# Kernel optimization log

Hardware: AMD Instinct MI355X
Metric: run time of the kernel (lower is better)

Reference implementation:

```python
import jax, jax.numpy as jnp
import numpy as np

D_MODEL = 512
N_LAYERS = 6
N_HEADS = 8
INNER = 2048
VOCAB = 2048
SEQ = 128
BATCH = 256
HEAD_DIM = D_MODEL // N_HEADS
EPS = 1e-5


def _pos_encoding(seq_len, d_model):
    pos = jnp.arange(seq_len, dtype=jnp.float32)[:, None]          # [S,1]
    i = jnp.arange(d_model // 2, dtype=jnp.float32)[None, :]       # [1,d/2]
    theta = pos / jnp.power(10000.0, 2.0 * i / d_model)            # [S,d/2]
    # interleave sin at even indices, cos at odd indices
    return jnp.stack([jnp.sin(theta), jnp.cos(theta)], axis=-1).reshape(seq_len, d_model)


def _layer_norm_2d(x):
    # F.layer_norm(x, (N, dims)): normalize over last TWO dims, no affine
    m = jnp.mean(x, axis=(1, 2), keepdims=True)
    v = jnp.mean(jnp.square(x - m), axis=(1, 2), keepdims=True)
    return (x - m) / jnp.sqrt(v + EPS)


def setup_inputs() -> dict:
    key = jax.random.key(0)
    ks = jax.random.split(key, 12)
    s = 0.02
    x = jax.random.randint(ks[0], (BATCH, SEQ), 0, VOCAB)
    emb = jax.random.normal(ks[1], (VOCAB, D_MODEL), jnp.float32) * s
    Wq = jax.random.normal(ks[2], (N_LAYERS, N_HEADS, D_MODEL, HEAD_DIM), jnp.float32) * s
    bq = jax.random.normal(ks[3], (N_LAYERS, N_HEADS, HEAD_DIM), jnp.float32) * s
    Wk = jax.random.normal(ks[4], (N_LAYERS, N_HEADS, D_MODEL, HEAD_DIM), jnp.float32) * s
    bk = jax.random.normal(ks[5], (N_LAYERS, N_HEADS, HEAD_DIM), jnp.float32) * s
    Wv = jax.random.normal(ks[6], (N_LAYERS, N_HEADS, D_MODEL, HEAD_DIM), jnp.float32) * s
    bv = jax.random.normal(ks[7], (N_LAYERS, N_HEADS, HEAD_DIM), jnp.float32) * s
    W1 = jax.random.normal(ks[8], (N_LAYERS, D_MODEL, INNER), jnp.float32) * s
    b1 = jax.random.normal(ks[9], (N_LAYERS, INNER), jnp.float32) * s
    W2 = jax.random.normal(ks[10], (N_LAYERS, INNER, D_MODEL), jnp.float32) * s
    b2 = jax.random.normal(ks[11], (N_LAYERS, D_MODEL), jnp.float32) * s
    return {"x": x, "emb": emb, "Wq": Wq, "bq": bq, "Wk": Wk, "bk": bk,
            "Wv": Wv, "bv": bv, "W1": W1, "b1": b1, "W2": W2, "b2": b2}


def reference(x, emb, Wq, bq, Wk, bk, Wv, bv, W1, b1, W2, b2):
    B, S = x.shape
    pe = _pos_encoding(SEQ, D_MODEL)
    h = emb[x] + pe[None, :, :]                                     # [B,S,D]
    scale = HEAD_DIM ** -0.5
    for l in range(N_LAYERS):
        q = jnp.einsum('bsd,hde->bhse', h, Wq[l]) + bq[l][None, :, None, :]
        k = jnp.einsum('bsd,hde->bhse', h, Wk[l]) + bk[l][None, :, None, :]
        v = jnp.einsum('bsd,hde->bhse', h, Wv[l]) + bv[l][None, :, None, :]
        scores = jnp.einsum('bhse,bhte->bhst', q, k) * scale        # no softmax!
        attn = jnp.einsum('bhst,bhte->bhse', scores, v)             # [B,H,S,E]
        attn = jnp.transpose(attn, (0, 2, 1, 3)).reshape(B, S, D_MODEL)
        h = _layer_norm_2d(h + attn)
        ff = jax.nn.relu(h @ W1[l] + b1[l]) @ W2[l] + b2[l]
        h = _layer_norm_2d(h + ff)
    return h
```

## Files before the change

kernel.cpp:

```cpp
#include <hip/hip_runtime.h>
#include <stdint.h>

#define NLAYERS 6
#define DMODEL  512
#define NHEADS  8
#define HDIM    64
#define INNER   2048
#define SEQ     128
#define BATCH   256
#define NTOK    (BATCH*SEQ)

typedef __attribute__((ext_vector_type(4))) float f32x4;
typedef __attribute__((ext_vector_type(8))) _Float16 hfrag;

typedef const __attribute__((address_space(1))) void* gas1p;
typedef __attribute__((address_space(3))) void* las3p;

__device__ __forceinline__ void load_lds16(const void* g, void* l) {
  __builtin_amdgcn_global_load_lds((gas1p)(uintptr_t)g, (las3p)(uint32_t)(uintptr_t)l, 16, 0, 0);
}

__device__ __forceinline__ ushort f2h(float f) {
  return __builtin_bit_cast(ushort, (_Float16)f);
}
__device__ __forceinline__ float h2f(ushort u) {
  return (float)__builtin_bit_cast(_Float16, u);
}

__device__ __forceinline__ f32x4 mfma16(hfrag a, hfrag b, f32x4 c) {
  return __builtin_amdgcn_mfma_f32_16x16x32_f16(a, b, c, 0, 0, 0);
}


__global__ void prep_qkv(const float* __restrict__ Wq, const float* __restrict__ Wk,
                         const float* __restrict__ Wv, const float* __restrict__ bq,
                         const float* __restrict__ bk, const float* __restrict__ bv,
                         ushort* __restrict__ Wt, float* __restrict__ biasq) {
  int idx = blockIdx.x*256 + threadIdx.x;
  if (idx >= NLAYERS*1536*512) return;
  const int k = idx & 511;
  const int n = (idx >> 9) % 1536;
  const int l = idx / (1536*512);
  const int which = n >> 9, hh = (n >> 6) & 7, e = n & 63;
  const float* W = (which == 0) ? Wq : ((which == 1) ? Wk : Wv);
  Wt[idx] = f2h(W[(((size_t)l*NHEADS + hh)*DMODEL + k)*HDIM + e]);
  if (k == 0) {
    const float* bb = (which == 0) ? bq : ((which == 1) ? bk : bv);
    biasq[l*1536 + n] = bb[((size_t)l*NHEADS + hh)*HDIM + e];
  }
}

__global__ void prep_w1(const float* __restrict__ W1, ushort* __restrict__ W1t) {
  int idx = blockIdx.x*256 + threadIdx.x;
  if (idx >= NLAYERS*INNER*512) return;
  const int k = idx & 511;
  const int n = (idx >> 9) % INNER;
  const int l = idx / (INNER*512);
  W1t[idx] = f2h(W1[((size_t)l*DMODEL + k)*INNER + n]);
}

__global__ void prep_w2(const float* __restrict__ W2, ushort* __restrict__ W2t) {
  int idx = blockIdx.x*256 + threadIdx.x;
  if (idx >= NLAYERS*512*INNER) return;
  const int k = idx & 2047;
  const int n = (idx >> 11) & 511;
  const int l = idx / (512*INNER);
  W2t[idx] = f2h(W2[((size_t)l*INNER + k)*DMODEL + n]);
}


__global__ void embed_kernel(const int* __restrict__ x, const float* __restrict__ emb,
                             ushort* __restrict__ hb) {
  const int t = blockIdx.x;
  const int i = threadIdx.x;
  const int s = t & (SEQ-1);
  const int tok = x[t];
  const float freq = expf(-(float)i * (9.210340371976184f / 256.0f));
  const float th = (float)s * freq;
  const float sn = sinf(th), cs = cosf(th);
  const size_t base = (size_t)t*DMODEL;
  const float v0 = emb[(size_t)tok*DMODEL + 2*i]     + sn;
  const float v1 = emb[(size_t)tok*DMODEL + 2*i + 1] + cs;
  *(uint*)(hb + base + 2*i) = (uint)f2h(v0) | ((uint)f2h(v1) << 16);
}


template<int K, int EPI>
__global__ __launch_bounds__(512, 2) void gemm256(
    const ushort* __restrict__ A, const ushort* __restrict__ Bt,
    const float* __restrict__ bias, ushort* __restrict__ outb,
    const int ldc, const int nbn) {
  __shared__ __align__(16) char lds[98304];
  constexpr int NKT = K / 32;
  constexpr int NG  = 2 * NKT;
  const int t = threadIdx.x;
  const int lane = t & 63, w = t >> 6;
  const int wr = w >> 2, wc = w & 3;
  const int cpx = (int)gridDim.x >> 3;
  const int wg  = ((int)blockIdx.x & 7) * cpx + ((int)blockIdx.x >> 3);
  const int bm = wg / nbn, bn = wg % nbn;

  const int fr = lane & 15;
  const int cxor = (((lane >> 4) ^ ((fr >> 1) & 3)) << 4);

  float bias_r[4];
  #pragma unroll
  for (int n = 0; n < 4; ++n) bias_r[n] = bias[bn*256 + wc*64 + n*16 + fr];
  asm volatile("" : "+v"(bias_r[0]), "+v"(bias_r[1]), "+v"(bias_r[2]), "+v"(bias_r[3]));

  const int srow = t >> 2;
  const int scc  = (t & 3) ^ ((t >> 3) & 3);
  const ushort* aSrc = A  + ((size_t)bm*256 + srow)*K + scc*8;
  const ushort* bSrc = Bt + ((size_t)bn*256 + srow)*K + scc*8;

  auto stage_g = [&](int g) {
    const int kt = g >> 1;
    const ushort* src = ((g & 1) ? bSrc : aSrc) + kt*32;
    char* dst = lds + (g % 6)*16384 + t*16;
    load_lds16(src, dst);
    load_lds16(src + (size_t)128*K, dst + 8192);
  };

  f32x4 acc[8][4] = {};

  stage_g(0); stage_g(1); stage_g(2); stage_g(3); stage_g(4);
  asm volatile("s_waitcnt vmcnt(6)" ::: "memory");
  __builtin_amdgcn_s_barrier();

  #pragma unroll 1
  for (int kt = 0; kt < NKT; ++kt) {
    const int Ab = ((2*kt) % 6) * 16384;
    hfrag a[8], b[4];
    #pragma unroll
    for (int m = 0; m < 8; ++m)
      a[m] = *(const hfrag*)(lds + Ab + (wr*128 + m*16 + fr)*64 + cxor);
    #pragma unroll
    for (int n = 0; n < 4; ++n)
      b[n] = *(const hfrag*)(lds + Ab + 16384 + (wc*64 + n*16 + fr)*64 + cxor);
    if (2*kt + 5 < NG) stage_g(2*kt + 5);
    __builtin_amdgcn_s_barrier();
    __builtin_amdgcn_s_setprio(1);
    #pragma unroll
    for (int m = 0; m < 4; ++m)
      #pragma unroll
      for (int n = 0; n < 4; ++n)
        acc[m][n] = mfma16(a[m], b[n], acc[m][n]);
    __builtin_amdgcn_s_setprio(0);
    __builtin_amdgcn_s_barrier();
    if (2*kt + 6 < NG) stage_g(2*kt + 6);
    __builtin_amdgcn_s_barrier();
    __builtin_amdgcn_s_setprio(1);
    #pragma unroll
    for (int m = 4; m < 8; ++m)
      #pragma unroll
      for (int n = 0; n < 4; ++n)
        acc[m][n] = mfma16(a[m], b[n], acc[m][n]);
    __builtin_amdgcn_s_setprio(0);
    if (kt < NKT - 3) {
      asm volatile("s_waitcnt vmcnt(6)" ::: "memory");
    } else if (kt == NKT - 3) {
      asm volatile("s_waitcnt vmcnt(4)" ::: "memory");
    } else if (kt == NKT - 2) {
      asm volatile("s_waitcnt vmcnt(0)" ::: "memory");
    }
    __builtin_amdgcn_s_barrier();
  }

  #pragma unroll
  for (int m = 0; m < 8; ++m) {
    #pragma unroll
    for (int n = 0; n < 4; ++n) {
      #pragma unroll
      for (int r4 = 0; r4 < 4; ++r4) {
        const int row = bm*256 + wr*128 + m*16 + ((lane >> 4) << 2) + r4;
        const int col = bn*256 + wc*64 + n*16 + fr;
        float v = acc[m][n][r4] + bias_r[n];
        if constexpr (EPI == 1) v = fmaxf(v, 0.0f);
        outb[(size_t)row*ldc + col] = f2h(v);
      }
    }
  }
}


__global__ __launch_bounds__(256) void attn_kernel(
    const ushort* __restrict__ qkv, ushort* __restrict__ outb) {
  __shared__ __align__(16) ushort wbuf[4][8192];
  const int tid = threadIdx.x;
  const int w = tid >> 6, lane = tid & 63;
  const int bh = blockIdx.x*4 + w;
  const int b = bh >> 3, h = bh & 7;
  const ushort* tokbase = qkv + (size_t)b*SEQ*1536;
  ushort* lds = &wbuf[w][0];
  ushort* kch = lds;
  ushort* vch = lds + 2048;

  f32x4 acc1[4][4] = {};
  #pragma unroll 1
  for (int sb = 0; sb < 4; ++sb) {
    const int s0 = sb*32;
    const int sr = lane >> 1;
    #pragma unroll
    for (int i = 0; i < 4; ++i) {
      const int cc  = i*2 + (lane & 1);
      const int ccs = cc ^ (sr & 7);
      const ushort* g = tokbase + (size_t)(s0+sr)*1536 + h*64 + cc*8;
      *(uint4*)(kch + sr*64 + ccs*8) = *(const uint4*)(g + 512);
      *(uint4*)(vch + sr*64 + ccs*8) = *(const uint4*)(g + 1024);
    }
    hfrag ak[4], av[4];
    #pragma unroll
    for (int m = 0; m < 4; ++m) {
      const int e1 = m*16 + (lane & 15);
      const int ccb = e1 >> 3, el = e1 & 7;
      #pragma unroll
      for (int j = 0; j < 8; ++j) {
        const int s = (lane >> 4)*8 + j;
        ak[m][j] = __builtin_bit_cast(_Float16, kch[s*64 + ((ccb ^ (s & 7))*8) + el]);
        av[m][j] = __builtin_bit_cast(_Float16, vch[s*64 + ((ccb ^ (s & 7))*8) + el]);
      }
    }
    #pragma unroll
    for (int m = 0; m < 4; ++m)
      #pragma unroll
      for (int n = 0; n < 4; ++n)
        acc1[m][n] = mfma16(ak[m], av[n], acc1[m][n]);
  }

  ushort* tv = lds;
  #pragma unroll
  for (int m = 0; m < 4; ++m)
    #pragma unroll
    for (int n = 0; n < 4; ++n)
      #pragma unroll
      for (int r4 = 0; r4 < 4; ++r4) {
        const int e1 = m*16 + (lane >> 4)*4 + r4;
        const int e2 = n*16 + (lane & 15);
        tv[e2*72 + e1] = f2h(acc1[m][n][r4] * 0.125f);
      }

  f32x4 acc2[8][4] = {};
  #pragma unroll
  for (int eb = 0; eb < 2; ++eb) {
    const int e1b = eb*32 + (lane >> 4)*8;
    hfrag aq[8], bk2[4];
    #pragma unroll
    for (int m = 0; m < 8; ++m) {
      const int s = m*16 + (lane & 15);
      aq[m] = *(const hfrag*)(tokbase + (size_t)s*1536 + h*64 + e1b);
    }
    #pragma unroll
    for (int n = 0; n < 4; ++n) {
      const int e2 = n*16 + (lane & 15);
      bk2[n] = *(const hfrag*)(tv + e2*72 + e1b);
    }
    #pragma unroll
    for (int m = 0; m < 8; ++m)
      #pragma unroll
      for (int n = 0; n < 4; ++n)
        acc2[m][n] = mfma16(aq[m], bk2[n], acc2[m][n]);
  }
  #pragma unroll
  for (int m = 0; m < 8; ++m)
    #pragma unroll
    for (int n = 0; n < 4; ++n)
      #pragma unroll
      for (int r4 = 0; r4 < 4; ++r4) {
        const int s  = m*16 + (lane >> 4)*4 + r4;
        const int e2 = n*16 + (lane & 15);
        outb[((size_t)b*SEQ + s)*DMODEL + h*HDIM + e2] = f2h(acc2[m][n][r4]);
      }
}


template<bool FINAL>
__global__ __launch_bounds__(1024) void resid_ln(
    const ushort* __restrict__ delta, ushort* __restrict__ hb, float* __restrict__ hf) {
  const int b = blockIdx.x;
  const size_t base = (size_t)b * (SEQ*DMODEL);
  uint4 cache[8];
  float s = 0.f, q = 0.f;
  #pragma unroll
  for (int j = 0; j < 8; ++j) {
    const size_t idx = base + (size_t)j*8192 + threadIdx.x*8;
    const uint4 hv = *(const uint4*)(hb + idx);
    const uint4 dv = *(const uint4*)(delta + idx);
    uint4 cv;
    #pragma unroll
    for (int c = 0; c < 4; ++c) {
      const uint hu = (&hv.x)[c], du = (&dv.x)[c];
      const float v0 = h2f((ushort)(hu & 0xffffu)) + h2f((ushort)(du & 0xffffu));
      const float v1 = h2f((ushort)(hu >> 16))     + h2f((ushort)(du >> 16));
      s += v0 + v1; q += v0*v0 + v1*v1;
      (&cv.x)[c] = (uint)f2h(v0) | ((uint)f2h(v1) << 16);
    }
    cache[j] = cv;
  }
  #pragma unroll
  for (int off = 32; off > 0; off >>= 1) {
    s += __shfl_down(s, off);
    q += __shfl_down(q, off);
  }
  __shared__ float ws_[16], wq_[16];
  __shared__ float stat[2];
  const int w = threadIdx.x >> 6, lane = threadIdx.x & 63;
  if (lane == 0) { ws_[w] = s; wq_[w] = q; }
  __syncthreads();
  if (threadIdx.x == 0) {
    float S = 0.f, Q = 0.f;
    #pragma unroll
    for (int i2 = 0; i2 < 16; ++i2) { S += ws_[i2]; Q += wq_[i2]; }
    const float mean = S * (1.0f/65536.0f);
    const float var  = Q * (1.0f/65536.0f) - mean*mean;
    stat[0] = mean; stat[1] = rsqrtf(var + 1e-5f);
  }
  __syncthreads();
  const float mean = stat[0], rstd = stat[1];
  #pragma unroll
  for (int j = 0; j < 8; ++j) {
    const size_t idx = base + (size_t)j*8192 + threadIdx.x*8;
    const uint4 cv = cache[j];
    if constexpr (FINAL) {
      #pragma unroll
      for (int c = 0; c < 4; ++c) {
        const uint u = (&cv.x)[c];
        const float o0 = (h2f((ushort)(u & 0xffffu)) - mean) * rstd;
        const float o1 = (h2f((ushort)(u >> 16))     - mean) * rstd;
        *(float2*)(hf + idx + c*2) = make_float2(o0, o1);
      }
    } else {
      uint4 ov;
      #pragma unroll
      for (int c = 0; c < 4; ++c) {
        const uint u = (&cv.x)[c];
        const float o0 = (h2f((ushort)(u & 0xffffu)) - mean) * rstd;
        const float o1 = (h2f((ushort)(u >> 16))     - mean) * rstd;
        (&ov.x)[c] = (uint)f2h(o0) | ((uint)f2h(o1) << 16);
      }
      *(uint4*)(hb + idx) = ov;
    }
  }
}


extern "C" void kernel_launch(void* const* d_in, const int* in_sizes, int n_in,
                              void* d_out, int out_size, void* d_ws, size_t ws_size,
                              hipStream_t stream) {
  const int*   x   = (const int*)d_in[0];
  const float* emb = (const float*)d_in[1];
  const float* Wq  = (const float*)d_in[2];
  const float* bq  = (const float*)d_in[3];
  const float* Wk  = (const float*)d_in[4];
  const float* bk  = (const float*)d_in[5];
  const float* Wv  = (const float*)d_in[6];
  const float* bv  = (const float*)d_in[7];
  const float* W1  = (const float*)d_in[8];
  const float* b1  = (const float*)d_in[9];
  const float* W2  = (const float*)d_in[10];
  const float* b2  = (const float*)d_in[11];
  float* h = (float*)d_out;

  char* p = (char*)d_ws;
  size_t off = 0;
  auto alloc = [&](size_t bytes) { char* r = p + off; off += (bytes + 255) & ~(size_t)255; return r; };
  ushort* Wqkv_t = (ushort*)alloc((size_t)NLAYERS*1536*512*2);
  ushort* W1t    = (ushort*)alloc((size_t)NLAYERS*INNER*512*2);
  ushort* W2t    = (ushort*)alloc((size_t)NLAYERS*512*INNER*2);
  float*  biasq  = (float*)alloc((size_t)NLAYERS*1536*4);
  ushort* hbf    = (ushort*)alloc((size_t)NTOK*512*2);
  ushort* big    = (ushort*)alloc((size_t)NTOK*2048*2);
  ushort* attnb  = (ushort*)alloc((size_t)NTOK*512*2);

  prep_qkv<<<(NLAYERS*1536*512 + 255)/256, 256, 0, stream>>>(Wq, Wk, Wv, bq, bk, bv, Wqkv_t, biasq);
  prep_w1<<<(NLAYERS*INNER*512 + 255)/256, 256, 0, stream>>>(W1, W1t);
  prep_w2<<<(NLAYERS*512*INNER + 255)/256, 256, 0, stream>>>(W2, W2t);
  embed_kernel<<<NTOK, 256, 0, stream>>>(x, emb, hbf);

  for (int l = 0; l < NLAYERS; ++l) {
    gemm256<512,0><<<768, 512, 0, stream>>>(
        hbf, Wqkv_t + (size_t)l*1536*512, biasq + (size_t)l*1536, big, 1536, 6);
    attn_kernel<<<BATCH*NHEADS/4, 256, 0, stream>>>(big, attnb);
    resid_ln<false><<<BATCH, 1024, 0, stream>>>(attnb, hbf, nullptr);
    gemm256<512,1><<<1024, 512, 0, stream>>>(
        hbf, W1t + (size_t)l*INNER*512, b1 + (size_t)l*INNER, big, 2048, 8);
    gemm256<2048,0><<<256, 512, 0, stream>>>(
        big, W2t + (size_t)l*512*INNER, b2 + (size_t)l*512, attnb, 512, 2);
    if (l == NLAYERS-1) {
      resid_ln<true><<<BATCH, 1024, 0, stream>>>(attnb, hbf, h);
    } else {
      resid_ln<false><<<BATCH, 1024, 0, stream>>>(attnb, hbf, nullptr);
    }
  }
}
```

Measured before the change: 1.812 ms.

## Shrink GEMM tile to 128x256 with 4 waves and double-buffered LDS

Replaces the 256x256 tile, 8-wave GEMM with a 128x256 tile run by 4 waves, where each wave covers all 128 rows and 64 columns. The 6-slot staged pipeline becomes a simple double buffer that halves LDS use, and the split MFMA phases are merged into one block of 32 MFMAs per k-step. This doubles the grid to improve occupancy and load balance across CUs and cuts barrier overhead. In exchange, each block reuses the B tile less, global traffic for B rises, and prefetch depth is shorter.

```diff
diff --git a/kernel.cpp b/kernel.cpp
--- a/kernel.cpp
+++ b/kernel.cpp
@@ -86,16 +86,14 @@
 
 
 template<int K, int EPI>
-__global__ __launch_bounds__(512, 2) void gemm256(
+__global__ __launch_bounds__(256, 2) void gemm_t(
     const ushort* __restrict__ A, const ushort* __restrict__ Bt,
     const float* __restrict__ bias, ushort* __restrict__ outb,
     const int ldc, const int nbn) {
-  __shared__ __align__(16) char lds[98304];
+  __shared__ __align__(16) char lds[49152];
   constexpr int NKT = K / 32;
-  constexpr int NG  = 2 * NKT;
   const int t = threadIdx.x;
-  const int lane = t & 63, w = t >> 6;
-  const int wr = w >> 2, wc = w & 3;
+  const int lane = t & 63, wc = t >> 6;
   const int cpx = (int)gridDim.x >> 3;
   const int wg  = ((int)blockIdx.x & 7) * cpx + ((int)blockIdx.x >> 3);
   const int bm = wg / nbn, bn = wg % nbn;
@@ -110,60 +108,51 @@
 
   const int srow = t >> 2;
   const int scc  = (t & 3) ^ ((t >> 3) & 3);
-  const ushort* aSrc = A  + ((size_t)bm*256 + srow)*K + scc*8;
+  const ushort* aSrc = A  + ((size_t)bm*128 + srow)*K + scc*8;
   const ushort* bSrc = Bt + ((size_t)bn*256 + srow)*K + scc*8;
 
-  auto stage_g = [&](int g) {
-    const int kt = g >> 1;
-    const ushort* src = ((g & 1) ? bSrc : aSrc) + kt*32;
-    char* dst = lds + (g % 6)*16384 + t*16;
-    load_lds16(src, dst);
-    load_lds16(src + (size_t)128*K, dst + 8192);
+  auto stage_t = [&](int j) {
+    char* dst = lds + (j & 1)*24576 + t*16;
+    const ushort* as = aSrc + j*32;
+    load_lds16(as,                  dst);
+    load_lds16(as + (size_t)64*K,   dst + 4096);
+    const ushort* bs = bSrc + j*32;
+    #pragma unroll
+    for (int i = 0; i < 4; ++i)
+      load_lds16(bs + (size_t)(i*64)*K, dst + 8192 + i*4096);
   };
 
   f32x4 acc[8][4] = {};
 
-  stage_g(0); stage_g(1); stage_g(2); stage_g(3); stage_g(4);
+  stage_t(0); stage_t(1);
   asm volatile("s_waitcnt vmcnt(6)" ::: "memory");
   __builtin_amdgcn_s_barrier();
 
   #pragma unroll 1
   for (int kt = 0; kt < NKT; ++kt) {
-    const int Ab = ((2*kt) % 6) * 16384;
+    const char* sl = lds + (kt & 1)*24576;
     hfrag a[8], b[4];
     #pragma unroll
     for (int m = 0; m < 8; ++m)
-      a[m] = *(const hfrag*)(lds + Ab + (wr*128 + m*16 + fr)*64 + cxor);
+      a[m] = *(const hfrag*)(sl + (m*16 + fr)*64 + cxor);
     #pragma unroll
     for (int n = 0; n < 4; ++n)
-      b[n] = *(const hfrag*)(lds + Ab + 16384 + (wc*64 + n*16 + fr)*64 + cxor);
-    if (2*kt + 5 < NG) stage_g(2*kt + 5);
-    __builtin_amdgcn_s_barrier();
+      b[n] = *(const hfrag*)(sl + 8192 + (wc*64 + n*16 + fr)*64 + cxor);
     __builtin_amdgcn_s_setprio(1);
     #pragma unroll
-    for (int m = 0; m < 4; ++m)
+    for (int m = 0; m < 8; ++m)
       #pragma unroll
       for (int n = 0; n < 4; ++n)
         acc[m][n] = mfma16(a[m], b[n], acc[m][n]);
     __builtin_amdgcn_s_setprio(0);
     __builtin_amdgcn_s_barrier();
-    if (2*kt + 6 < NG) stage_g(2*kt + 6);
+    if (kt + 2 < NKT) {
+      stage_t(kt + 2);
+      asm volatile("s_waitcnt vmcnt(6)" ::: "memory");
+    } else if (kt + 2 == NKT) {
+      asm volatile("s_waitcnt vmcnt(0)" ::: "memory");
+    }
     __builtin_amdgcn_s_barrier();
-    __builtin_amdgcn_s_setprio(1);
-    #pragma unroll
-    for (int m = 4; m < 8; ++m)
-      #pragma unroll
-      for (int n = 0; n < 4; ++n)
-        acc[m][n] = mfma16(a[m], b[n], acc[m][n]);
-    __builtin_amdgcn_s_setprio(0);
-    if (kt < NKT - 3) {
-      asm volatile("s_waitcnt vmcnt(6)" ::: "memory");
-    } else if (kt == NKT - 3) {
-      asm volatile("s_waitcnt vmcnt(4)" ::: "memory");
-    } else if (kt == NKT - 2) {
-      asm volatile("s_waitcnt vmcnt(0)" ::: "memory");
-    }
-    __builtin_amdgcn_s_barrier();
   }
 
   #pragma unroll
@@ -172,7 +161,7 @@
     for (int n = 0; n < 4; ++n) {
       #pragma unroll
       for (int r4 = 0; r4 < 4; ++r4) {
-        const int row = bm*256 + wr*128 + m*16 + ((lane >> 4) << 2) + r4;
+        const int row = bm*128 + m*16 + ((lane >> 4) << 2) + r4;
         const int col = bn*256 + wc*64 + n*16 + fr;
         float v = acc[m][n][r4] + bias_r[n];
         if constexpr (EPI == 1) v = fmaxf(v, 0.0f);
@@ -377,13 +366,13 @@
   embed_kernel<<<NTOK, 256, 0, stream>>>(x, emb, hbf);
 
   for (int l = 0; l < NLAYERS; ++l) {
-    gemm256<512,0><<<768, 512, 0, stream>>>(
+    gemm_t<512,0><<<1536, 256, 0, stream>>>(
         hbf, Wqkv_t + (size_t)l*1536*512, biasq + (size_t)l*1536, big, 1536, 6);
     attn_kernel<<<BATCH*NHEADS/4, 256, 0, stream>>>(big, attnb);
     resid_ln<false><<<BATCH, 1024, 0, stream>>>(attnb, hbf, nullptr);
-    gemm256<512,1><<<1024, 512, 0, stream>>>(
+    gemm_t<512,1><<<2048, 256, 0, stream>>>(
         hbf, W1t + (size_t)l*INNER*512, b1 + (size_t)l*INNER, big, 2048, 8);
-    gemm256<2048,0><<<256, 512, 0, stream>>>(
+    gemm_t<2048,0><<<512, 256, 0, stream>>>(
         big, W2t + (size_t)l*512*INNER, b2 + (size_t)l*512, attnb, 512, 2);
     if (l == NLAYERS-1) {
       resid_ln<true><<<BATCH, 1024, 0, stream>>>(attnb, hbf, h);
```

Result: no change. 1.825 ms (+0.7%).
